# Performance work log

Measured on AMD Instinct MI355X. Metric: run time of the kernel, lower is better.

Reference implementation:

```python
import jax, jax.numpy as jnp
import numpy as np

N_WAY = 5
K_SHOT = 1
PROJ_DIM = 64
TEMPERATURE = 0.2
EPS_COS = 1e-12   # F.normalize eps in InnerproductSimilarity (cosine)
EPS_L2 = 1e-16    # _l2norm eps


def setup_inputs() -> dict:
    key = jax.random.key(0)
    ks = jax.random.split(key, 8)
    b, q, u, c, h, w = 2, 15, 20, 64, 21, 21
    s = N_WAY * K_SHOT
    std = float(np.sqrt(2.0 / PROJ_DIM))  # kaiming init used for 1x1 conv heads
    return {
        "support_xf": jax.random.normal(ks[0], (b, s, c, h, w), jnp.float32),
        "support_y": jax.random.randint(ks[1], (b, s), 0, N_WAY),
        "query_xf": jax.random.normal(ks[2], (b, q, c, h, w), jnp.float32),
        "query_y": jax.random.randint(ks[3], (b, q), 0, N_WAY),
        "unlabeled_xf": jax.random.normal(ks[4], (b, u, c, h, w), jnp.float32),
        "key_w": jax.random.normal(ks[5], (PROJ_DIM, c), jnp.float32) * std,
        "query_w": jax.random.normal(ks[6], (PROJ_DIM, c), jnp.float32) * std,
        "value_w": jax.random.normal(ks[7], (PROJ_DIM, c), jnp.float32) * std,
    }


def _dual_nn_selection(support_xf, unlabeled_xf):
    """Mutual-NN (dual NN) selection of unlabeled positions per class.
    Returns padded gather indices idx [b,n_way,L], 0/1 validity sel [b,n_way,L], and L.
    L is data-dependent (max per-(batch,class) count), computed eagerly like the
    original torch code's umask_length."""
    b, u, c, h, w = unlabeled_xf.shape
    M_u, M_s = u * h * w, K_SHOT * h * w
    unl = jnp.transpose(unlabeled_xf, (0, 2, 1, 3, 4)).reshape(b, c, M_u)  # [b,c,M_u]
    sup = jnp.transpose(support_xf.reshape(b, N_WAY, K_SHOT, c, h, w), (0, 1, 3, 2, 4, 5)).reshape(b, N_WAY, c, M_s)
    # cosine InnerproductSimilarity: normalize over channel dim
    sup_n = sup / jnp.maximum(jnp.linalg.norm(sup, axis=2, keepdims=True), EPS_COS)
    unl_n = unl / jnp.maximum(jnp.linalg.norm(unl, axis=1, keepdims=True), EPS_COS)
    u2s = jnp.einsum('bcm,bncs->bnms', unl_n, sup_n)  # [b,n_way,M_u,M_s]
    flat = jnp.transpose(u2s, (0, 2, 1, 3)).reshape(b, M_u, N_WAY * M_s)
    s_near = jnp.argmax(flat, axis=1)   # [b, n_way*M_s] nearest unlabeled pos per support slot
    u_near = jnp.argmax(flat, axis=2)   # [b, M_u] nearest support slot per unlabeled pos
    mutual = (jnp.take_along_axis(s_near, u_near, axis=1) == jnp.arange(M_u)[None, :])  # [b,M_u]
    cls = jnp.argmax(jnp.max(u2s, axis=-1), axis=1)  # [b,M_u] class assignment
    umask = jnp.transpose(jax.nn.one_hot(cls, N_WAY, dtype=jnp.float32), (0, 2, 1)) \
            * mutual[:, None, :].astype(jnp.float32)  # [b,n_way,M_u]
    L = int(jnp.max(jnp.sum(umask, axis=-1)))  # umask_length (data-dependent)
    order = jnp.argsort(-umask, axis=-1)       # stable: selected positions first, original order
    idx = order[:, :, :L]                      # [b,n_way,L]
    sel = jnp.take_along_axis(umask, idx, axis=-1)  # 1 = real feature, 0 = zero padding
    return idx, sel, L


def _forward_core(support_xf, query_xf, unlabeled_xf, key_w, query_w, value_w, query_y, idx, sel):
    b, q, c, h, w = query_xf.shape
    hw = h * w
    u = unlabeled_xf.shape[1]
    M_u, M_s = u * hw, K_SHOT * hw
    unl = jnp.transpose(unlabeled_xf, (0, 2, 1, 3, 4)).reshape(b, c, M_u)
    sup = jnp.transpose(support_xf.reshape(b, N_WAY, K_SHOT, c, h, w), (0, 1, 3, 2, 4, 5)).reshape(b, N_WAY, c, M_s)
    # ragged per-class scatter realized as padded gather (zeros where sel==0)
    gathered = jnp.take_along_axis(unl[:, None, :, :], idx[:, :, None, :], axis=-1)  # [b,n_way,c,L]
    unl_dual = gathered * sel[:, :, None, :]
    s_cat_u = jnp.concatenate([sup, unl_dual], axis=-1)  # [b,n_way,c,M_s+L]
    # 1x1 conv heads == channel matmuls
    qf = query_xf.reshape(b, q, c, hw)
    q_proj = jnp.einsum('oc,bqcm->bqom', query_w, qf)   # [b,q,64,hw]
    v_query = jnp.einsum('oc,bqcm->bqom', value_w, qf)  # [b,q,64,hw]
    k_sup = jnp.einsum('oc,bncl->bnol', key_w, s_cat_u)
    v_sup = jnp.einsum('oc,bncl->bnol', value_w, s_cat_u)
    simi = jnp.einsum('bqom,bnol->bqnml', q_proj, k_sup) / np.float32(np.sqrt(PROJ_DIM))  # [b,q,n,hw,Ms+L]
    Lt = simi.shape[-1]
    # _MNN with compensate_for_single == False (encoder == 'FourLayer_64F')
    merged = jnp.transpose(simi, (0, 1, 3, 2, 4)).reshape(b, q, hw, N_WAY * Lt)
    q_near = jnp.argmax(merged, axis=-1)  # [b,q,hw]
    s_near = jnp.argmax(merged, axis=-2)  # [b,q,n_way*Lt]
    q_mask = (jnp.take_along_axis(s_near, q_near, axis=-1) == jnp.arange(hw)[None, None, :]).astype(simi.dtype)
    att = jax.nn.softmax(simi * q_mask[:, :, None, :, None], axis=-1)
    aligned = jnp.einsum('bqnml,bnol->bqnmo', att, v_sup)  # [b,q,n_way,hw,64]
    aligned = aligned / (jnp.linalg.norm(aligned, axis=-1, keepdims=True) + EPS_L2)
    vq = v_query / (jnp.linalg.norm(v_query, axis=2, keepdims=True) + EPS_L2)
    simi2 = (jnp.einsum('bqnmo,bqok->bqnmk', aligned, vq) + 1.0) * 0.5  # FourLayer_64F rescale
    logits = jnp.sum(jnp.max(simi2, axis=-2), axis=-1).reshape(b * q, N_WAY)  # topk(1,-2)+mean == max
    logp = jax.nn.log_softmax(logits / np.float32(TEMPERATURE), axis=-1)
    y = query_y.reshape(b * q)
    return -jnp.mean(jnp.take_along_axis(logp, y[:, None], axis=1))  # CrossEntropyLoss


def reference(support_xf, support_y, query_xf, query_y, unlabeled_xf, key_w, query_w, value_w):
    idx, sel, _ = _dual_nn_selection(support_xf, unlabeled_xf)
    return _forward_core(support_xf, query_xf, unlabeled_xf, key_w, query_w, value_w, query_y, idx, sel)
```

## Files before the change

### kernel.cpp

```cpp
#include <hip/hip_runtime.h>
#include <math.h>

#define B 2
#define Q 15
#define U 20
#define C 64
#define HW 441
#define NW 5
#define MU (U*HW)
#define MS HW
#define NJ (NW*MS)
#define PD 64
#define LCAP NJ
#define LTCAP 896
#define SCAP 896
#define MSP 448
#define NEGF (-3.402823466e38f)

__device__ float g_rnu[B*MU];
__device__ float g_rns[B*NJ];
__device__ unsigned long long g_snearpack[B*NJ];
__device__ unsigned long long g_unearpack[B*MU];
__device__ int   g_counts[B*NW];
__device__ int   g_L[1];
__device__ int   g_selidx[B*NW*LCAP];
__device__ float g_ksup[(size_t)B*NW*PD*LTCAP];
__device__ float g_vsup[(size_t)B*NW*PD*LTCAP];
__device__ float g_vsupT[(size_t)B*NW*LTCAP*PD];
__device__ float g_vbarn[B*NW*PD];
__device__ float g_qproj[(size_t)B*Q*PD*MSP];
__device__ float g_vqn[(size_t)B*Q*PD*MSP];
__device__ unsigned long long g_rowpack[(size_t)B*Q*NW*MSP];
__device__ unsigned long long g_snear2pack[(size_t)B*Q*NW*LTCAP];
__device__ int   g_qmrows[B*Q*MSP];
__device__ int   g_qmcount[B*Q];
__device__ unsigned g_cmax[(size_t)B*Q*NW*MSP];
__device__ float g_logits[B*Q*NW];
__device__ float g_scores[(size_t)B*Q*NW*MSP*SCAP];

__device__ __forceinline__ unsigned enc_f(float f){
  unsigned b=__float_as_uint(f);
  return (b&0x80000000u)? ~b : (b|0x80000000u);
}
__device__ __forceinline__ float dec_f(unsigned k){
  unsigned b=(k&0x80000000u)?(k^0x80000000u):~k;
  return __uint_as_float(b);
}
__device__ __forceinline__ unsigned long long pk_make(float v,int idx){
  return ((unsigned long long)enc_f(v)<<32)|(unsigned)~(unsigned)idx;
}
__device__ __forceinline__ int pk_idx(unsigned long long p){
  return (int)~(unsigned)(p&0xFFFFFFFFull);
}

__global__ void k_init(){
  int i=blockIdx.x*256+threadIdx.x;
  if (i<B*NJ) g_snearpack[i]=0ull;
  if (i<B*MU) g_unearpack[i]=0ull;
  if (i<B*Q*NW*MSP){ g_rowpack[i]=0ull; g_cmax[i]=0u; }
  if (i<B*Q*NW*LTCAP) g_snear2pack[i]=0ull;
  if (i==0) g_L[0]=0;
}

__global__ void k_norms(const float* __restrict__ sup, const float* __restrict__ unl){
  int i=blockIdx.x*256+threadIdx.x;
  if (i<B*MU){
    int b=i/MU, m=i%MU, ui=m/HW, p=m%HW;
    const float* base=unl+((size_t)(b*U+ui)*C)*HW+p;
    float ss=0.f;
    for (int c=0;c<C;c++){ float x=base[(size_t)c*HW]; ss+=x*x; }
    g_rnu[i]=1.f/fmaxf(sqrtf(ss),1e-12f);
  }
  if (i<B*NJ){
    int b=i/NJ, j=i%NJ, n=j/MS, s=j%MS;
    const float* base=sup+((size_t)(b*NW+n)*C)*HW+s;
    float ss=0.f;
    for (int c=0;c<C;c++){ float x=base[(size_t)c*HW]; ss+=x*x; }
    g_rns[i]=1.f/fmaxf(sqrtf(ss),1e-12f);
  }
}

__global__ __launch_bounds__(256) void k_u2s(const float* __restrict__ sup, const float* __restrict__ unl){
  int blk=blockIdx.x;
  int grp=blk%6; blk/=6;
  int rb=blk%138; int b=blk/138;
  int mb=rb*64;
  int tid=threadIdx.x, tm=tid>>4, tl=tid&15;
  int lane=tid&63, w=tid>>6;
  __shared__ __align__(16) float Ut[4096];
  __shared__ __align__(16) float Pt[8192];
  __shared__ unsigned long long colred[512];
  int mv=min(64,MU-mb);
  for (int k=tid;k<4096;k+=256){
    int c=k>>6, mm=k&63; float v=0.f;
    if (mm<mv){ int m=mb+mm, ui=m/HW, p=m%HW; v=unl[((size_t)(b*U+ui)*C+c)*HW+p]*g_rnu[b*MU+m]; }
    Ut[c*64+mm]=v;
  }
  unsigned long long rowpk[4]={0ull,0ull,0ull,0ull};
  for (int t=0;t<3;t++){
    int j0=(grp*3+t)*128;
    int jv=min(128,NJ-j0);
    __syncthreads();
    for (int k=tid;k<8192;k+=256){
      int c=k>>7, jj=k&127; float v=0.f;
      if (jj<jv){ int j=j0+jj, n=j/MS, s=j%MS; v=sup[((size_t)(b*NW+n)*C+c)*HW+s]*g_rns[b*NJ+j]; }
      Pt[c*128+jj]=v;
    }
    __syncthreads();
    float s[4][8]={};
    for (int c=0;c<64;c++){
      float a[4],b0[4],b1[4];
      *(float4*)a =*(const float4*)&Ut[c*64+tm*4];
      *(float4*)b0=*(const float4*)&Pt[c*128+tl*4];
      *(float4*)b1=*(const float4*)&Pt[c*128+64+tl*4];
      #pragma unroll
      for (int i=0;i<4;i++)
        #pragma unroll
        for (int j=0;j<4;j++){ s[i][j]=fmaf(a[i],b0[j],s[i][j]); s[i][j+4]=fmaf(a[i],b1[j],s[i][j+4]); }
    }
    #pragma unroll
    for (int i=0;i<4;i++){
      if (tm*4+i<mv){
        unsigned long long p=rowpk[i];
        #pragma unroll
        for (int j=0;j<8;j++){
          int jj=(j<4)?(tl*4+j):(64+tl*4+(j-4));
          if (jj<jv){
            unsigned long long c2=pk_make(s[i][j],j0+jj);
            if (c2>p) p=c2;
          }
        }
        rowpk[i]=p;
      }
    }
    unsigned long long cpk[8];
    #pragma unroll
    for (int j=0;j<8;j++){
      unsigned long long p=0ull;
      #pragma unroll
      for (int i=0;i<4;i++){
        if (tm*4+i<mv){
          unsigned long long c2=pk_make(s[i][j],mb+tm*4+i);
          if (c2>p) p=c2;
        }
      }
      cpk[j]=p;
    }
    #pragma unroll
    for (int j=0;j<8;j++){
      unsigned long long o;
      o=__shfl_xor(cpk[j],16); if (o>cpk[j]) cpk[j]=o;
      o=__shfl_xor(cpk[j],32); if (o>cpk[j]) cpk[j]=o;
    }
    if ((lane>>4)==0){
      #pragma unroll
      for (int j=0;j<8;j++){
        int jj=(j<4)?(tl*4+j):(64+tl*4+(j-4));
        colred[w*128+jj]=cpk[j];
      }
    }
    __syncthreads();
    if (tid<128 && tid<jv){
      unsigned long long p=colred[tid];
      if (colred[128+tid]>p) p=colred[128+tid];
      if (colred[256+tid]>p) p=colred[256+tid];
      if (colred[384+tid]>p) p=colred[384+tid];
      if (p) atomicMax(&g_snearpack[b*NJ+j0+tid],p);
    }
  }
  #pragma unroll
  for (int i=0;i<4;i++){
    unsigned long long p=rowpk[i];
    #pragma unroll
    for (int mk=1;mk<16;mk<<=1){ unsigned long long o=__shfl_xor(p,mk); if (o>p) p=o; }
    if (tl==0 && tm*4+i<mv && p) atomicMax(&g_unearpack[b*MU+mb+tm*4+i],p);
  }
}

__global__ __launch_bounds__(256) void k_compact(){
  int b=blockIdx.x/NW, n=blockIdx.x%NW;
  int tid=threadIdx.x, lane=tid&63, w=tid>>6;
  __shared__ int wtot[4];
  int base=0;
  for (int m0=0;m0<MU;m0+=256){
    int m=m0+tid;
    bool flag=false;
    if (m<MU){
      int j=pk_idx(g_unearpack[b*MU+m]);
      flag=(j/MS==n) && (pk_idx(g_snearpack[b*NJ+j])==m);
    }
    unsigned long long bal=__ballot(flag);
    if (lane==0) wtot[w]=(int)__popcll(bal);
    __syncthreads();
    int wpre=0, tot=0;
    #pragma unroll
    for (int ww=0;ww<4;ww++){ if (ww<w) wpre+=wtot[ww]; tot+=wtot[ww]; }
    if (flag){
      int pre=(int)__popcll(bal&((1ull<<lane)-1ull));
      g_selidx[(b*NW+n)*LCAP+base+wpre+pre]=m;
    }
    base+=tot;
    __syncthreads();
  }
  if (tid==0){ g_counts[b*NW+n]=base; atomicMax(&g_L[0],base); }
}

__global__ __launch_bounds__(256) void k_kv(const float* __restrict__ sup, const float* __restrict__ unl,
                                            const float* __restrict__ kw, const float* __restrict__ vw){
  int blk=blockIdx.x;
  int lb=blk%(LTCAP/64); blk/=(LTCAP/64);
  int n=blk%NW, b=blk/NW;
  int Lt=MS+g_L[0];
  if (lb*64>=Lt) return;
  int cnt=g_counts[b*NW+n];
  int tid=threadIdx.x, lane=tid&63, w=tid>>6;
  __shared__ float F[4096];
  __shared__ const float* ptr_s[64];
  if (tid<64){
    int l=lb*64+tid;
    const float* p=nullptr;
    if (l<MS) p=&sup[((size_t)(b*NW+n)*C)*HW+l];
    else if (l<MS+cnt){
      int mg=g_selidx[(b*NW+n)*LCAP+(l-MS)];
      int ui=mg/HW, pp=mg%HW;
      p=&unl[((size_t)(b*U+ui)*C)*HW+pp];
    }
    ptr_s[tid]=p;
  }
  __syncthreads();
  for (int k=tid;k<4096;k+=256){
    int c=k>>6, ll=k&63;
    const float* p=ptr_s[ll];
    F[c*64+ll]=p?p[(size_t)c*HW]:0.f;
  }
  __syncthreads();
  int l=lb*64+lane;
  size_t ob=((size_t)(b*NW+n)*PD)*LTCAP+l;
  size_t tb=((size_t)(b*NW+n)*LTCAP+l)*PD;
  for (int oo=0;oo<16;oo++){
    int o=w*16+oo;
    float ka=0.f, va=0.f;
    for (int c=0;c<C;c++){ float f=F[c*64+lane]; ka=fmaf(kw[o*C+c],f,ka); va=fmaf(vw[o*C+c],f,va); }
    g_ksup[ob+(size_t)o*LTCAP]=ka;
    g_vsup[ob+(size_t)o*LTCAP]=va;
    g_vsupT[tb+o]=va;
  }
}

__global__ __launch_bounds__(256) void k_vbar(){
  int bn=blockIdx.x;
  int tid=threadIdx.x, lane=tid&63, w=tid>>6;
  int cnt=g_counts[bn];
  int Lt=MS+g_L[0];
  __shared__ float vb_s[64];
  for (int oo=0;oo<16;oo++){
    int o=w*16+oo;
    const float* row=&g_vsup[((size_t)bn*PD+o)*LTCAP];
    float s=0.f;
    for (int l=lane;l<MS+cnt;l+=64) s+=row[l];
    #pragma unroll
    for (int mk=1;mk<64;mk<<=1) s+=__shfl_xor(s,mk);
    if (lane==0) vb_s[o]=s/(float)Lt;
  }
  __syncthreads();
  if (tid<64){
    float v=vb_s[tid];
    float ss=v*v;
    #pragma unroll
    for (int mk=1;mk<64;mk<<=1) ss+=__shfl_xor(ss,mk);
    g_vbarn[bn*PD+tid]=v/(sqrtf(ss)+1e-16f);
  }
}

__global__ __launch_bounds__(256) void k_qproj(const float* __restrict__ qx, const float* __restrict__ qw,
                                               const float* __restrict__ vw){
  int blk=blockIdx.x;
  int mt=blk%7; blk/=7;
  int bq=blk;
  int tid=threadIdx.x, lane=tid&63, w=tid>>6;
  __shared__ float F[4096];
  __shared__ float ssp[256];
  for (int k=tid;k<4096;k+=256){
    int c=k>>6, mm=k&63, m=mt*64+mm;
    F[c*64+mm]=(m<MS)?qx[((size_t)bq*C+c)*HW+m]:0.f;
  }
  __syncthreads();
  int m=mt*64+lane;
  size_t ob=(size_t)bq*PD*MSP+m;
  float va[16]; float ssl=0.f;
  for (int oo=0;oo<16;oo++){
    int o=w*16+oo;
    float qa=0.f, v=0.f;
    for (int c=0;c<C;c++){ float f=F[c*64+lane]; qa=fmaf(qw[o*C+c],f,qa); v=fmaf(vw[o*C+c],f,v); }
    g_qproj[ob+(size_t)o*MSP]=qa;
    va[oo]=v; ssl=fmaf(v,v,ssl);
  }
  ssp[tid]=ssl;
  __syncthreads();
  float ss=ssp[lane]+ssp[64+lane]+ssp[128+lane]+ssp[192+lane];
  float rn=1.f/(sqrtf(ss)+1e-16f);
  for (int oo=0;oo<16;oo++) g_vqn[ob+(size_t)(w*16+oo)*MSP]=va[oo]*rn;
}

__global__ __launch_bounds__(256) void k_passA(){
  int blk=blockIdx.x;
  int mh=blk%4; blk/=4;
  int n=blk%NW; blk/=NW;
  int bq=blk; int b=bq/Q;
  int Lt=MS+g_L[0];
  int nch=(Lt+63)>>6;
  int tid=threadIdx.x, tm=tid>>4, tl=tid&15;
  int lane=tid&63, w=tid>>6;
  int bqn=bq*NW+n;
  int m0=mh*128;
  __shared__ __align__(16) float Qt[8192];
  __shared__ __align__(16) float Kt[4096];
  __shared__ unsigned long long colred[256];
  const size_t qb=(size_t)bq*PD*MSP;
  const size_t kb=(size_t)(b*NW+n)*PD*LTCAP;
  for (int k=tid;k<2048;k+=256){
    int o=k>>5, mq=k&31;
    int m=m0+mq*4;
    float4 v=make_float4(0.f,0.f,0.f,0.f);
    if (m<MSP) v=*(const float4*)&g_qproj[qb+(size_t)o*MSP+m];
    *(float4*)&Qt[o*128+mq*4]=v;
  }
  unsigned long long rowpk[8]={0ull,0ull,0ull,0ull,0ull,0ull,0ull,0ull};
  for (int lc=0;lc<nch;lc++){
    int l0=lc<<6, lv=min(64,Lt-l0);
    __syncthreads();
    for (int k=tid;k<1024;k+=256){
      int o=k>>4, lq=k&15;
      *(float4*)&Kt[o*64+lq*4]=*(const float4*)&g_ksup[kb+(size_t)o*LTCAP+l0+lq*4];
    }
    __syncthreads();
    float s[8][4]={};
    for (int c=0;c<64;c++){
      float a[8],bv[4];
      *(float4*)&a[0]=*(const float4*)&Qt[c*128+tm*8];
      *(float4*)&a[4]=*(const float4*)&Qt[c*128+tm*8+4];
      *(float4*)bv=*(const float4*)&Kt[c*64+tl*4];
      #pragma unroll
      for (int i=0;i<8;i++)
        #pragma unroll
        for (int j=0;j<4;j++) s[i][j]=fmaf(a[i],bv[j],s[i][j]);
    }
    #pragma unroll
    for (int i=0;i<8;i++)
      #pragma unroll
      for (int j=0;j<4;j++) s[i][j]*=0.125f;
    #pragma unroll
    for (int i=0;i<8;i++){
      int m=m0+tm*8+i;
      if (m<MS)
        *(float4*)&g_scores[((size_t)bqn*MSP+m)*SCAP+l0+tl*4]
            =make_float4(s[i][0],s[i][1],s[i][2],s[i][3]);
    }
    #pragma unroll
    for (int i=0;i<8;i++){
      int m=m0+tm*8+i;
      if (m<MS){
        unsigned long long p=rowpk[i];
        #pragma unroll
        for (int j=0;j<4;j++){
          if (tl*4+j<lv){
            unsigned long long c2=pk_make(s[i][j],l0+tl*4+j);
            if (c2>p) p=c2;
          }
        }
        rowpk[i]=p;
      }
    }
    unsigned long long cpk[4];
    #pragma unroll
    for (int j=0;j<4;j++){
      unsigned long long p=0ull;
      #pragma unroll
      for (int i=0;i<8;i++){
        int m=m0+tm*8+i;
        if (m<MS){
          unsigned long long c2=pk_make(s[i][j],m);
          if (c2>p) p=c2;
        }
      }
      cpk[j]=p;
    }
    #pragma unroll
    for (int j=0;j<4;j++){
      unsigned long long o;
      o=__shfl_xor(cpk[j],16); if (o>cpk[j]) cpk[j]=o;
      o=__shfl_xor(cpk[j],32); if (o>cpk[j]) cpk[j]=o;
    }
    if ((lane>>4)==0){
      #pragma unroll
      for (int j=0;j<4;j++) colred[w*64+tl*4+j]=cpk[j];
    }
    __syncthreads();
    if (tid<64 && tid<lv){
      unsigned long long p=colred[tid];
      if (colred[64+tid]>p) p=colred[64+tid];
      if (colred[128+tid]>p) p=colred[128+tid];
      if (colred[192+tid]>p) p=colred[192+tid];
      if (p) atomicMax(&g_snear2pack[(size_t)bqn*LTCAP+l0+tid],p);
    }
  }
  #pragma unroll
  for (int i=0;i<8;i++){
    int m=m0+tm*8+i;
    unsigned long long p=rowpk[i];
    #pragma unroll
    for (int mk=1;mk<16;mk<<=1){ unsigned long long o=__shfl_xor(p,mk); if (o>p) p=o; }
    if (tl==0 && m<MS && p) atomicMax(&g_rowpack[(size_t)bqn*MSP+m],p);
  }
}

__global__ __launch_bounds__(256) void k_qmask(){
  int bq=blockIdx.x;
  int tid=threadIdx.x, lane=tid&63, w=tid>>6;
  __shared__ int wtot[4];
  int base=0;
  for (int m0=0;m0<MS;m0+=256){
    int m=m0+tid;
    bool qm=false;
    if (m<MS){
      unsigned bhv=0u; unsigned long long bp=0ull; int bn=0;
      #pragma unroll
      for (int n=0;n<NW;n++){
        unsigned long long pk=g_rowpack[(size_t)(bq*NW+n)*MSP+m];
        unsigned hv=(unsigned)(pk>>32);
        if (hv>bhv){bhv=hv;bp=pk;bn=n;}
      }
      int bl=pk_idx(bp);
      qm=(pk_idx(g_snear2pack[(size_t)(bq*NW+bn)*LTCAP+bl])==m);
    }
    unsigned long long bal=__ballot(qm);
    if (lane==0) wtot[w]=(int)__popcll(bal);
    __syncthreads();
    int wpre=0, tot=0;
    #pragma unroll
    for (int ww=0;ww<4;ww++){ if (ww<w) wpre+=wtot[ww]; tot+=wtot[ww]; }
    if (qm){
      int pre=(int)__popcll(bal&((1ull<<lane)-1ull));
      g_qmrows[bq*MSP+base+wpre+pre]=m;
    }
    base+=tot;
    __syncthreads();
  }
  if (tid==0) g_qmcount[bq]=base;
}

__global__ __launch_bounds__(256) void k_passB(){
  int blk=blockIdx.x;
  int rt=blk%7; blk/=7;
  int n=blk%NW; blk/=NW;
  int bq=blk; int b=bq/Q;
  int nm=g_qmcount[bq];
  if (rt*64>=nm) return;
  int bqn=bq*NW+n;
  int Lt=MS+g_L[0];
  int nch=(Lt+63)>>6;
  int tid=threadIdx.x, tm=tid>>4, tl=tid&15;
  __shared__ __align__(16) float Vt[4096];
  __shared__ __align__(16) float Pt[64*68];
  __shared__ int rows_s[64];
  if (tid<64){ int g=rt*64+tid; rows_s[tid]=(g<nm)?g_qmrows[bq*MSP+g]:0; }
  __syncthreads();
  float rmax[4]; size_t sb[4];
  #pragma unroll
  for (int i=0;i<4;i++){
    int row=rows_s[tm*4+i];
    rmax[i]=dec_f((unsigned)(g_rowpack[(size_t)bqn*MSP+row]>>32));
    sb[i]=((size_t)bqn*MSP+row)*SCAP;
  }
  const size_t vb=(size_t)(b*NW+n)*LTCAP*PD;
  const size_t qb=(size_t)bq*PD*MSP;
  float lsum[4]={0.f,0.f,0.f,0.f};
  float acc[4][4]={};
  for (int lc=0;lc<nch;lc++){
    int l0=lc<<6, lv=min(64,Lt-l0);
    __syncthreads();
    float4 sv[4];
    #pragma unroll
    for (int i=0;i<4;i++) sv[i]=*(const float4*)&g_scores[sb[i]+l0+tl*4];
    {
      const float* src=&g_vsupT[vb+(size_t)l0*PD];
      #pragma unroll
      for (int it=0;it<4;it++){
        int f4=tid+it*256;
        *(float4*)&Vt[f4*4]=*(const float4*)&src[f4*4];
      }
    }
    #pragma unroll
    for (int i=0;i<4;i++){
      float e0=(tl*4+0<lv)?__expf(sv[i].x-rmax[i]):0.f;
      float e1=(tl*4+1<lv)?__expf(sv[i].y-rmax[i]):0.f;
      float e2=(tl*4+2<lv)?__expf(sv[i].z-rmax[i]):0.f;
      float e3=(tl*4+3<lv)?__expf(sv[i].w-rmax[i]):0.f;
      lsum[i]+=(e0+e1)+(e2+e3);
      *(float4*)&Pt[(tm*4+i)*68+tl*4]=make_float4(e0,e1,e2,e3);
    }
    __syncthreads();
    for (int l4=0;l4<64;l4+=4){
      float4 pq[4];
      #pragma unroll
      for (int i=0;i<4;i++) pq[i]=*(const float4*)&Pt[(tm*4+i)*68+l4];
      #pragma unroll
      for (int u=0;u<4;u++){
        float4 v4=*(const float4*)&Vt[(l4+u)*64+tl*4];
        #pragma unroll
        for (int i=0;i<4;i++){
          float p=((const float*)&pq[i])[u];
          acc[i][0]=fmaf(p,v4.x,acc[i][0]);
          acc[i][1]=fmaf(p,v4.y,acc[i][1]);
          acc[i][2]=fmaf(p,v4.z,acc[i][2]);
          acc[i][3]=fmaf(p,v4.w,acc[i][3]);
        }
      }
    }
  }
  float rn[4];
  #pragma unroll
  for (int i=0;i<4;i++){
    float ls=lsum[i];
    #pragma unroll
    for (int mk=1;mk<16;mk<<=1) ls+=__shfl_xor(ls,mk);
    float ss=0.f;
    #pragma unroll
    for (int j=0;j<4;j++){ acc[i][j]/=ls; ss=fmaf(acc[i][j],acc[i][j],ss); }
    #pragma unroll
    for (int mk=1;mk<16;mk<<=1) ss+=__shfl_xor(ss,mk);
    rn[i]=1.f/(sqrtf(ss)+1e-16f);
  }
  __syncthreads();
  #pragma unroll
  for (int i=0;i<4;i++)
    *(float4*)&Pt[(tm*4+i)*68+tl*4]=make_float4(acc[i][0],acc[i][1],acc[i][2],acc[i][3]);
  int rowok[4];
  #pragma unroll
  for (int i=0;i<4;i++) rowok[i]=(rt*64+tm*4+i<nm);
  for (int kt=0;kt<7;kt++){
    __syncthreads();
    for (int k=tid;k<1024;k+=256){
      int o=k>>4, kq=k&15;
      *(float4*)&Vt[o*64+kq*4]=*(const float4*)&g_vqn[qb+(size_t)o*MSP+kt*64+kq*4];
    }
    __syncthreads();
    float d[4][4]={};
    for (int o=0;o<64;o++){
      float a[4], bv4[4];
      #pragma unroll
      for (int i=0;i<4;i++) a[i]=Pt[(tm*4+i)*68+o];
      *(float4*)bv4=*(const float4*)&Vt[o*64+tl*4];
      #pragma unroll
      for (int i=0;i<4;i++)
        #pragma unroll
        for (int j=0;j<4;j++) d[i][j]=fmaf(a[i],bv4[j],d[i][j]);
    }
    #pragma unroll
    for (int j=0;j<4;j++){
      int kg=kt*64+tl*4+j;
      float mv=NEGF;
      #pragma unroll
      for (int i=0;i<4;i++) if (rowok[i]) mv=fmaxf(mv,d[i][j]*rn[i]);
      mv=fmaxf(mv,__shfl_xor(mv,16));
      mv=fmaxf(mv,__shfl_xor(mv,32));
      if (((tid>>4)&3)==0 && kg<MS && mv>-1e37f)
        atomicMax(&g_cmax[(size_t)bqn*MSP+kg],enc_f(mv));
    }
  }
}

__global__ __launch_bounds__(256) void k_logits(){
  int bqn=blockIdx.x;
  int n=bqn%NW, bq=bqn/NW, b=bq/Q;
  int tid=threadIdx.x;
  int nm=g_qmcount[bq];
  __shared__ float red[256];
  __shared__ float vb_s[64];
  if (tid<64) vb_s[tid]=g_vbarn[(b*NW+n)*PD+tid];
  __syncthreads();
  const float* vq=&g_vqn[(size_t)bq*PD*MSP];
  float p=0.f;
  for (int k=tid;k<MS;k+=256){
    float v=dec_f(g_cmax[(size_t)bqn*MSP+k]);
    if (nm<MS){
      float d=0.f;
      for (int o=0;o<PD;o++) d=fmaf(vb_s[o],vq[(size_t)o*MSP+k],d);
      v=fmaxf(v,d);
    }
    p+=(v+1.f)*0.5f;
  }
  red[tid]=p; __syncthreads();
  for (int s=128;s;s>>=1){ if (tid<s) red[tid]+=red[tid+s]; __syncthreads(); }
  if (tid==0) g_logits[bqn]=red[0];
}

__global__ void k_loss(const int* __restrict__ qy, float* __restrict__ out){
  int t=threadIdx.x;
  float lp=0.f;
  if (t<B*Q){
    int y=qy[t];
    float xv[NW]; float mxv=NEGF;
    #pragma unroll
    for (int n=0;n<NW;n++){ xv[n]=g_logits[t*NW+n]*5.f; mxv=fmaxf(mxv,xv[n]); }
    float s=0.f, xy=0.f;
    #pragma unroll
    for (int n=0;n<NW;n++){ s+=__expf(xv[n]-mxv); if (n==y) xy=xv[n]; }
    lp=xy-mxv-logf(s);
  }
  #pragma unroll
  for (int off=32;off;off>>=1) lp+=__shfl_down(lp,off);
  if (t==0) out[0]=-lp/(float)(B*Q);
}

extern "C" void kernel_launch(void* const* d_in, const int* in_sizes, int n_in,
                              void* d_out, int out_size, void* d_ws, size_t ws_size,
                              hipStream_t stream) {
  (void)in_sizes; (void)n_in; (void)out_size; (void)d_ws; (void)ws_size;
  const float* sup=(const float*)d_in[0];
  const float* qx =(const float*)d_in[2];
  const int*   qy =(const int*)d_in[3];
  const float* unl=(const float*)d_in[4];
  const float* kw =(const float*)d_in[5];
  const float* qw =(const float*)d_in[6];
  const float* vw =(const float*)d_in[7];
  float* out=(float*)d_out;

  k_init   <<<525,256,0,stream>>>();
  k_norms  <<<69,256,0,stream>>>(sup,unl);
  k_u2s    <<<B*138*6,256,0,stream>>>(sup,unl);
  k_compact<<<B*NW,256,0,stream>>>();
  k_kv     <<<B*NW*(LTCAP/64),256,0,stream>>>(sup,unl,kw,vw);
  k_vbar   <<<B*NW,256,0,stream>>>();
  k_qproj  <<<B*Q*7,256,0,stream>>>(qx,qw,vw);
  k_passA  <<<B*Q*NW*4,256,0,stream>>>();
  k_qmask  <<<B*Q,256,0,stream>>>();
  k_passB  <<<B*Q*NW*7,256,0,stream>>>();
  k_logits <<<B*Q*NW,256,0,stream>>>();
  k_loss   <<<1,64,0,stream>>>(qy,out);
}
```

Before: 755.9 us.

## Split passA over L chunks across blocks with wider 128-column tiles

k_passA previously had each block loop serially over all 64-wide L chunks. Now each block handles one 128-wide L chunk, using an 8x8 register tile per thread, and the grid grows sevenfold, with early exit for unused chunks. The aim is more parallelism across the GPU (the old grid was 600 blocks) and less serial looping per block. In exchange, each block reloads the Q tile and issues more row-max atomics to global memory. Register pressure also rises with the larger accumulator tile.

After: 759.6 us. Within noise of the previous version (+0.5%).

```diff
diff --git a/kernel.cpp b/kernel.cpp
--- a/kernel.cpp
+++ b/kernel.cpp
@@ -304,113 +304,100 @@
 
 __global__ __launch_bounds__(256) void k_passA(){
   int blk=blockIdx.x;
+  int lc=blk%7; blk/=7;
   int mh=blk%4; blk/=4;
   int n=blk%NW; blk/=NW;
   int bq=blk; int b=bq/Q;
   int Lt=MS+g_L[0];
-  int nch=(Lt+63)>>6;
+  int nch=(Lt+127)>>7;
+  if (lc>=nch) return;
+  int l0=lc<<7, lv=min(128,Lt-l0);
   int tid=threadIdx.x, tm=tid>>4, tl=tid&15;
   int lane=tid&63, w=tid>>6;
   int bqn=bq*NW+n;
   int m0=mh*128;
   __shared__ __align__(16) float Qt[8192];
-  __shared__ __align__(16) float Kt[4096];
-  __shared__ unsigned long long colred[256];
+  __shared__ __align__(16) float Kt[8192];
+  __shared__ unsigned long long colred[512];
   const size_t qb=(size_t)bq*PD*MSP;
   const size_t kb=(size_t)(b*NW+n)*PD*LTCAP;
-  for (int k=tid;k<2048;k+=256){
-    int o=k>>5, mq=k&31;
+  for (int k4=tid;k4<2048;k4+=256){
+    int o=k4>>5, mq=k4&31;
     int m=m0+mq*4;
     float4 v=make_float4(0.f,0.f,0.f,0.f);
     if (m<MSP) v=*(const float4*)&g_qproj[qb+(size_t)o*MSP+m];
     *(float4*)&Qt[o*128+mq*4]=v;
-  }
-  unsigned long long rowpk[8]={0ull,0ull,0ull,0ull,0ull,0ull,0ull,0ull};
-  for (int lc=0;lc<nch;lc++){
-    int l0=lc<<6, lv=min(64,Lt-l0);
-    __syncthreads();
-    for (int k=tid;k<1024;k+=256){
-      int o=k>>4, lq=k&15;
-      *(float4*)&Kt[o*64+lq*4]=*(const float4*)&g_ksup[kb+(size_t)o*LTCAP+l0+lq*4];
-    }
-    __syncthreads();
-    float s[8][4]={};
-    for (int c=0;c<64;c++){
-      float a[8],bv[4];
-      *(float4*)&a[0]=*(const float4*)&Qt[c*128+tm*8];
-      *(float4*)&a[4]=*(const float4*)&Qt[c*128+tm*8+4];
-      *(float4*)bv=*(const float4*)&Kt[c*64+tl*4];
-      #pragma unroll
-      for (int i=0;i<8;i++)
-        #pragma unroll
-        for (int j=0;j<4;j++) s[i][j]=fmaf(a[i],bv[j],s[i][j]);
-    }
+    *(float4*)&Kt[o*128+mq*4]=*(const float4*)&g_ksup[kb+(size_t)o*LTCAP+l0+mq*4];
+  }
+  __syncthreads();
+  float s[8][8]={};
+  for (int c=0;c<64;c++){
+    float a[8],b0[4],b1[4];
+    *(float4*)&a[0]=*(const float4*)&Qt[c*128+tm*8];
+    *(float4*)&a[4]=*(const float4*)&Qt[c*128+tm*8+4];
+    *(float4*)b0=*(const float4*)&Kt[c*128+tl*4];
+    *(float4*)b1=*(const float4*)&Kt[c*128+64+tl*4];
     #pragma unroll
     for (int i=0;i<8;i++)
       #pragma unroll
-      for (int j=0;j<4;j++) s[i][j]*=0.125f;
-    #pragma unroll
-    for (int i=0;i<8;i++){
-      int m=m0+tm*8+i;
-      if (m<MS)
-        *(float4*)&g_scores[((size_t)bqn*MSP+m)*SCAP+l0+tl*4]
-            =make_float4(s[i][0],s[i][1],s[i][2],s[i][3]);
-    }
+      for (int j=0;j<4;j++){ s[i][j]=fmaf(a[i],b0[j],s[i][j]); s[i][j+4]=fmaf(a[i],b1[j],s[i][j+4]); }
+  }
+  #pragma unroll
+  for (int i=0;i<8;i++)
+    #pragma unroll
+    for (int j=0;j<8;j++) s[i][j]*=0.125f;
+  #pragma unroll
+  for (int i=0;i<8;i++){
+    int m=m0+tm*8+i;
+    if (m<MS){
+      size_t sbase=((size_t)bqn*MSP+m)*SCAP+l0;
+      *(float4*)&g_scores[sbase+tl*4]   =make_float4(s[i][0],s[i][1],s[i][2],s[i][3]);
+      *(float4*)&g_scores[sbase+64+tl*4]=make_float4(s[i][4],s[i][5],s[i][6],s[i][7]);
+    }
+  }
+  #pragma unroll
+  for (int i=0;i<8;i++){
+    int m=m0+tm*8+i;
+    unsigned long long p=0ull;
+    if (m<MS){
+      #pragma unroll
+      for (int j=0;j<8;j++){
+        int jj=(j<4)?(tl*4+j):(64+tl*4+(j-4));
+        if (jj<lv){
+          unsigned long long c2=pk_make(s[i][j],l0+jj);
+          if (c2>p) p=c2;
+        }
+      }
+    }
+    #pragma unroll
+    for (int mk=1;mk<16;mk<<=1){ unsigned long long o=__shfl_xor(p,mk); if (o>p) p=o; }
+    if (tl==0 && m<MS && p) atomicMax(&g_rowpack[(size_t)bqn*MSP+m],p);
+  }
+  #pragma unroll
+  for (int j=0;j<8;j++){
+    int jj=(j<4)?(tl*4+j):(64+tl*4+(j-4));
+    unsigned long long p=0ull;
     #pragma unroll
     for (int i=0;i<8;i++){
       int m=m0+tm*8+i;
       if (m<MS){
-        unsigned long long p=rowpk[i];
-        #pragma unroll
-        for (int j=0;j<4;j++){
-          if (tl*4+j<lv){
-            unsigned long long c2=pk_make(s[i][j],l0+tl*4+j);
-            if (c2>p) p=c2;
-          }
-        }
-        rowpk[i]=p;
-      }
-    }
-    unsigned long long cpk[4];
-    #pragma unroll
-    for (int j=0;j<4;j++){
-      unsigned long long p=0ull;
-      #pragma unroll
-      for (int i=0;i<8;i++){
-        int m=m0+tm*8+i;
-        if (m<MS){
-          unsigned long long c2=pk_make(s[i][j],m);
-          if (c2>p) p=c2;
-        }
-      }
-      cpk[j]=p;
-    }
-    #pragma unroll
-    for (int j=0;j<4;j++){
-      unsigned long long o;
-      o=__shfl_xor(cpk[j],16); if (o>cpk[j]) cpk[j]=o;
-      o=__shfl_xor(cpk[j],32); if (o>cpk[j]) cpk[j]=o;
-    }
-    if ((lane>>4)==0){
-      #pragma unroll
-      for (int j=0;j<4;j++) colred[w*64+tl*4+j]=cpk[j];
-    }
-    __syncthreads();
-    if (tid<64 && tid<lv){
-      unsigned long long p=colred[tid];
-      if (colred[64+tid]>p) p=colred[64+tid];
-      if (colred[128+tid]>p) p=colred[128+tid];
-      if (colred[192+tid]>p) p=colred[192+tid];
-      if (p) atomicMax(&g_snear2pack[(size_t)bqn*LTCAP+l0+tid],p);
-    }
-  }
-  #pragma unroll
-  for (int i=0;i<8;i++){
-    int m=m0+tm*8+i;
-    unsigned long long p=rowpk[i];
-    #pragma unroll
-    for (int mk=1;mk<16;mk<<=1){ unsigned long long o=__shfl_xor(p,mk); if (o>p) p=o; }
-    if (tl==0 && m<MS && p) atomicMax(&g_rowpack[(size_t)bqn*MSP+m],p);
+        unsigned long long c2=pk_make(s[i][j],m);
+        if (c2>p) p=c2;
+      }
+    }
+    {
+      unsigned long long o=__shfl_xor(p,16); if (o>p) p=o;
+      o=__shfl_xor(p,32); if (o>p) p=o;
+    }
+    if ((lane>>4)==0) colred[w*128+jj]=p;
+  }
+  __syncthreads();
+  if (tid<128 && tid<lv){
+    unsigned long long p=colred[tid];
+    if (colred[128+tid]>p) p=colred[128+tid];
+    if (colred[256+tid]>p) p=colred[256+tid];
+    if (colred[384+tid]>p) p=colred[384+tid];
+    if (p) atomicMax(&g_snear2pack[(size_t)bqn*LTCAP+l0+tid],p);
   }
 }
 
@@ -633,7 +620,7 @@
   k_kv     <<<B*NW*(LTCAP/64),256,0,stream>>>(sup,unl,kw,vw);
   k_vbar   <<<B*NW,256,0,stream>>>();
   k_qproj  <<<B*Q*7,256,0,stream>>>(qx,qw,vw);
-  k_passA  <<<B*Q*NW*4,256,0,stream>>>();
+  k_passA  <<<B*Q*NW*28,256,0,stream>>>();
   k_qmask  <<<B*Q,256,0,stream>>>();
   k_passB  <<<B*Q*NW*7,256,0,stream>>>();
   k_logits <<<B*Q*NW,256,0,stream>>>();
```
